# Kernel tuning notes

Measured on AMD Instinct MI355X. Metric: run time of the kernel, lower is better.

## Reference

```python
import jax, jax.numpy as jnp
import numpy as np

N, E, H, G, L = 50000, 640000, 128, 8, 3

def setup_inputs() -> dict:
    key = jax.random.key(0)
    ks = jax.random.split(key, 10)
    s = 1.0 / np.sqrt(H)
    return {
        "x": jax.random.normal(ks[0], (N, H), jnp.float32),
        "query": jax.random.normal(ks[1], (G, H), jnp.float32),
        "Wl": jax.random.normal(ks[2], (L, H, H), jnp.float32) * s,
        "bl": jax.random.normal(ks[3], (L, H), jnp.float32) * s,
        "Wr": jax.random.normal(ks[4], (L, H, H), jnp.float32) * s,
        "Wlin": jax.random.normal(ks[5], (H, H), jnp.float32) * s,
        "blin": jax.random.normal(ks[6], (H,), jnp.float32) * s,
        "edge_index": jax.random.randint(ks[7], (2, E), 0, N, jnp.int64),
        "batch_vec": jnp.sort(jax.random.randint(ks[8], (N,), 0, G, jnp.int64)),
    }

def reference(x, query, Wl, bl, Wr, Wlin, blin, edge_index, batch_vec):
    src, dst = edge_index[0], edge_index[1]
    n = x.shape[0]
    for i in range(L):
        # SAGEConv(aggr='max'): gather neighbor feats, scatter-max to dst
        m = jax.ops.segment_max(x[src], dst, num_segments=n)  # [N,H]
        m = jnp.where(jnp.isfinite(m), m, 0.0)  # isolated nodes -> 0 (PyG)
        x = jax.nn.relu(m @ Wl[i].T + bl[i] + x @ Wr[i].T)
    x = x @ Wlin.T + blin  # encoder final linear
    # cosine scoring per graph, vectorized via batch_vec
    xn = x / jnp.linalg.norm(x, axis=1, keepdims=True).clip(1e-12)
    qn = query / jnp.linalg.norm(query, axis=1, keepdims=True).clip(1e-12)
    scores = jnp.sum(xn * qn[batch_vec], axis=1)  # [N]
    return scores
```

## Files before the change

### kernel.cpp

```cpp
#include <hip/hip_runtime.h>
#include <math.h>

#define H 128

typedef _Float16 half8 __attribute__((ext_vector_type(8)));
typedef float f32x16 __attribute__((ext_vector_type(16)));
typedef int int4v __attribute__((ext_vector_type(4)));

__device__ __forceinline__ half8 h8max(half8 a, half8 b) {
#if defined(__has_builtin) && __has_builtin(__builtin_elementwise_max)
    return __builtin_elementwise_max(a, b);
#else
    half8 r;
#pragma unroll
    for (int j = 0; j < 8; ++j) r[j] = a[j] > b[j] ? a[j] : b[j];
    return r;
#endif
}

__device__ __forceinline__ half8 h8shfl_xor(half8 v, int mask) {
    int4v iv;
    __builtin_memcpy(&iv, &v, 16);
#pragma unroll
    for (int j = 0; j < 4; ++j) iv[j] = __shfl_xor(iv[j], mask, 64);
    half8 r;
    __builtin_memcpy(&r, &iv, 16);
    return r;
}


__global__ __launch_bounds__(256) void scan_atomic(const int* __restrict__ deg,
                                                   int* __restrict__ offsets,
                                                   int* __restrict__ gcur, int N) {
    __shared__ int buf[256];
    __shared__ int sbase;
    int tid = threadIdx.x;
    int i = blockIdx.x * 256 + tid;
    int v = (i < N) ? deg[i] : 0;
    int incl = v;
    buf[tid] = v;
    __syncthreads();
#pragma unroll
    for (int off = 1; off < 256; off <<= 1) {
        int t = (tid >= off) ? buf[tid - off] : 0;
        __syncthreads();
        incl += t;
        buf[tid] = incl;
        __syncthreads();
    }
    if (tid == 255) sbase = atomicAdd(gcur, incl);
    __syncthreads();
    if (i < N) offsets[i] = sbase + incl - v;
}

__global__ __launch_bounds__(256) void fill_adj(const int* __restrict__ ei, int E,
                                                const int* __restrict__ offsets,
                                                int* __restrict__ cursor,
                                                int* __restrict__ adj) {
    int e = blockIdx.x * 256 + threadIdx.x;
    if (e < E) {
        int s = ei[e];
        int d = ei[E + e];
        int pos = atomicAdd(&cursor[d], 1);
        adj[offsets[d] + pos] = s;
    }
}


__global__ __launch_bounds__(256) void prep_all(
    const int* __restrict__ ei, int E, int* __restrict__ deg,
    const float* __restrict__ x, const float* __restrict__ query,
    const float* __restrict__ Wl, const float* __restrict__ Wr,
    const float* __restrict__ Wlin, _Float16* __restrict__ xh,
    _Float16* __restrict__ wimg, float* __restrict__ qn, int n8, int HB, int SB,
    int WB) {
    int b = blockIdx.x;
    int tid = threadIdx.x;
    if (b < HB) {
        int e = b * 256 + tid;
        if (e < E) atomicAdd(&deg[ei[E + e]], 1);
    } else if (b < HB + SB) {
        int i = (b - HB) * 256 + tid;
        if (i < n8) {
            const float4* x4 = (const float4*)x;
            float4 u = x4[(size_t)i * 2], v = x4[(size_t)i * 2 + 1];
            float f[8] = {u.x, u.y, u.z, u.w, v.x, v.y, v.z, v.w};
            half8 h;
#pragma unroll
            for (int j = 0; j < 8; ++j) h[j] = (_Float16)f[j];
            *(half8*)(xh + (size_t)i * 8) = h;
        }
    } else if (b < HB + SB + WB) {
        int gidx = (b - HB - SB) * 256 + tid;
        if (gidx < 7 * 2048) {
            int mat = gidx / 2048;
            int rem = gidx - mat * 2048;
            int n = rem >> 4;
            int g = rem & 15;
            const float* src = (mat == 6) ? Wlin
                             : ((mat & 1) ? Wr + (mat >> 1) * H * H
                                          : Wl + (mat >> 1) * H * H);
            const float* p = src + n * H + g * 8;
            half8 h, l;
#pragma unroll
            for (int j = 0; j < 8; ++j) {
                float v = p[j];
                _Float16 hh = (_Float16)v;
                h[j] = hh;
                l[j] = (_Float16)(v - (float)hh);
            }
            int kc4 = g >> 2, gpc = g & 3;
            int posB = (gpc + (n & 3) + ((n >> 2) & 3)) & 3;
            size_t base = (size_t)mat * 32768 + (size_t)kc4 * 8192 + n * 32 + posB * 8;
            *(half8*)(wimg + base) = h;
            *(half8*)(wimg + base + 4096) = l;
        }
    } else {
        int g = b - HB - SB - WB;
        __shared__ float part[4];
        float v = (tid < 128) ? query[g * H + tid] : 0.f;
        float ss = v * v;
#pragma unroll
        for (int off = 32; off > 0; off >>= 1) ss += __shfl_xor(ss, off, 64);
        if ((tid & 63) == 0) part[tid >> 6] = ss;
        __syncthreads();
        float tot = part[0] + part[1];
        if (tid < 128) qn[g * H + tid] = v / fmaxf(sqrtf(tot), 1e-12f);
    }
}


__global__ __launch_bounds__(256, 8) void layer_fused(
    const half8* __restrict__ Xh, const int* __restrict__ deg,
    const int* __restrict__ offsets, const int* __restrict__ adj,
    const _Float16* __restrict__ Bimg, const float* __restrict__ bias,
    _Float16* __restrict__ Yh, int N) {
    __shared__ __align__(16) _Float16 sU[4096];

    int tid = threadIdx.x;
    int w = tid >> 6;
    int lane = tid & 63;
    int l31 = lane & 31;
    int lhi = lane >> 5;
    int n0 = blockIdx.x * 32;

    {
        int sub = lane >> 4;
        int lf = lane & 15;
        const _Float16 ni = (_Float16)(-INFINITY);
        const half8 ninf = {ni, ni, ni, ni, ni, ni, ni, ni};
        const half8 hz = {(_Float16)0.f, (_Float16)0.f, (_Float16)0.f, (_Float16)0.f,
                          (_Float16)0.f, (_Float16)0.f, (_Float16)0.f, (_Float16)0.f};
        int nd = n0 + w * 8 + (lf & 7);
        int ndc = nd < N ? nd : N - 1;
        int e0v = offsets[ndc];
        int degv = (nd < N) ? deg[ndc] : 0;

        int dmx = degv;
#pragma unroll
        for (int off = 1; off <= 8; off <<= 1) {
            int t = __shfl_xor(dmx, off, 64);
            dmx = t > dmx ? t : dmx;
        }

        if (dmx <= 32) {
            int adjf[4];
#pragma unroll
            for (int rr = 0; rr < 4; ++rr) {
                int i = 2 * rr + (lane >> 5);
                int e0 = __shfl(e0v, i, 64);
                int d = __shfl(degv, i, 64);
                int s = lane & 31;
                int p = d > 0 ? e0 + (s < d ? s : d - 1) : 0;
                adjf[rr] = adj[p];
            }
#pragma unroll
            for (int i = 0; i < 8; ++i) {
                int d = __shfl(degv, i, 64);
                int dm1 = d > 0 ? d - 1 : 0;
                half8 v[8];
#pragma unroll
                for (int q = 0; q < 8; ++q) {
                    int j = q * 4 + sub;
                    int jc = j < d ? j : dm1;
                    int idx = __shfl(adjf[i >> 1], ((i & 1) << 5) | jc, 64);
                    v[q] = Xh[(size_t)idx * 16 + lf];
                }
                half8 acc = h8max(h8max(h8max(v[0], v[1]), h8max(v[2], v[3])),
                                  h8max(h8max(v[4], v[5]), h8max(v[6], v[7])));
                acc = h8max(acc, h8shfl_xor(acc, 16));
                acc = h8max(acc, h8shfl_xor(acc, 32));
                if (d == 0) acc = hz;
                int row = w * 8 + i;
                if (sub == 0) *(half8*)&sU[row * 128 + ((lf ^ (row & 15)) << 3)] = acc;
            }
        } else {
            for (int i = 0; i < 8; ++i) {
                int e0 = __shfl(e0v, i, 64);
                int d = __shfl(degv, i, 64);
                int row = w * 8 + i;
                half8 acc = ninf;
                for (int base = 0; base < d; base += 16) {
                    half8 v[4];
#pragma unroll
                    for (int q = 0; q < 4; ++q) {
                        int j = base + q * 4 + sub;
                        int idx = adj[e0 + (j < d ? j : d - 1)];
                        v[q] = Xh[(size_t)idx * 16 + lf];
                    }
                    acc = h8max(acc, h8max(h8max(v[0], v[1]), h8max(v[2], v[3])));
                }
                acc = h8max(acc, h8shfl_xor(acc, 16));
                acc = h8max(acc, h8shfl_xor(acc, 32));
                if (d == 0) acc = hz;
                if (sub == 0) *(half8*)&sU[row * 128 + ((lf ^ (row & 15)) << 3)] = acc;
            }
        }
    }
    __syncthreads();

    f32x16 acc;
    {
        float bvv = bias[w * 32 + l31];
#pragma unroll
        for (int r = 0; r < 16; ++r) acc[r] = bvv;
    }

    int rl = l31;
    int n = w * 32 + l31;

#pragma unroll
    for (int kc4 = 0; kc4 < 4; ++kc4) {
        const _Float16* Bc = Bimg + (size_t)kc4 * 8192;
#pragma unroll
        for (int ks = 0; ks < 2; ++ks) {
            int g16 = kc4 * 4 + ks * 2 + lhi;
            int posA = g16 ^ (rl & 15);
            half8 ah = *(const half8*)&sU[rl * 128 + posA * 8];
            int gpc = ks * 2 + lhi;
            int posB = (gpc + (n & 3) + ((n >> 2) & 3)) & 3;
            half8 bh = *(const half8*)&Bc[n * 32 + posB * 8];
            half8 bl2 = *(const half8*)&Bc[4096 + n * 32 + posB * 8];
            acc = __builtin_amdgcn_mfma_f32_32x32x16_f16(ah, bh, acc, 0, 0, 0);
            acc = __builtin_amdgcn_mfma_f32_32x32x16_f16(ah, bl2, acc, 0, 0, 0);
        }
    }

#pragma unroll
    for (int kc64 = 0; kc64 < 2; ++kc64) {
        __syncthreads();
        {
            int row = tid >> 3;
            int gp8 = tid & 7;
            int nn = n0 + row;
            half8 h = {(_Float16)0.f, (_Float16)0.f, (_Float16)0.f, (_Float16)0.f,
                       (_Float16)0.f, (_Float16)0.f, (_Float16)0.f, (_Float16)0.f};
            if (nn < N) h = Xh[(size_t)nn * 16 + kc64 * 8 + gp8];
            int pos8 = (gp8 + (row & 7) + ((row >> 3) & 7)) & 7;
            *(half8*)&sU[row * 72 + pos8 * 8] = h;
        }
        __syncthreads();
#pragma unroll
        for (int kc4 = 2 * kc64; kc4 < 2 * kc64 + 2; ++kc4) {
            const _Float16* Bc = Bimg + 32768 + (size_t)kc4 * 8192;
#pragma unroll
            for (int ks = 0; ks < 2; ++ks) {
                int gp8 = (kc4 & 1) * 4 + ks * 2 + lhi;
                int posA8 = (gp8 + (rl & 7) + ((rl >> 3) & 7)) & 7;
                half8 ah = *(const half8*)&sU[rl * 72 + posA8 * 8];
                int gpc = ks * 2 + lhi;
                int posB = (gpc + (n & 3) + ((n >> 2) & 3)) & 3;
                half8 bh = *(const half8*)&Bc[n * 32 + posB * 8];
                half8 bl2 = *(const half8*)&Bc[4096 + n * 32 + posB * 8];
                acc = __builtin_amdgcn_mfma_f32_32x32x16_f16(ah, bh, acc, 0, 0, 0);
                acc = __builtin_amdgcn_mfma_f32_32x32x16_f16(ah, bl2, acc, 0, 0, 0);
            }
        }
    }

#pragma unroll
    for (int r = 0; r < 16; ++r) {
        int row = n0 + (r & 3) + 8 * (r >> 2) + 4 * lhi;
        if (row < N) Yh[(size_t)row * H + n] = (_Float16)fmaxf(acc[r], 0.f);
    }
}


__global__ __launch_bounds__(256) void final_mfma6(
    const half8* __restrict__ Xh, const _Float16* __restrict__ Bimg,
    const float* __restrict__ blin, const float* __restrict__ qn,
    const int* __restrict__ bv, float* __restrict__ out, int N) {
    __shared__ __align__(16) _Float16 sA[9216];
    __shared__ __align__(16) _Float16 sB[8192];

    int tid = threadIdx.x;
    int w = tid >> 6;
    int lane = tid & 63;
    int l31 = lane & 31;
    int lhi = lane >> 5;
    int n0 = blockIdx.x * 128;

    int arow = n0 + w * 32 + l31;
    arow = arow < N ? arow : N - 1;
    int gl = bv[arow];

    f32x16 acc[4];
#pragma unroll
    for (int nt = 0; nt < 4; ++nt) {
        float b = blin[nt * 32 + l31];
#pragma unroll
        for (int r = 0; r < 16; ++r) acc[nt][r] = b;
    }

    int rl = w * 32 + l31;

    for (int kc4 = 0; kc4 < 4; ++kc4) {
        if (kc4) __syncthreads();
        {
            const half8* bsrc = (const half8*)(Bimg + (size_t)kc4 * 8192);
            half8* bdst = (half8*)sB;
#pragma unroll
            for (int i = 0; i < 4; ++i) bdst[tid + i * 256] = bsrc[tid + i * 256];
        }
        if ((kc4 & 1) == 0) {
            int kc64 = kc4 >> 1;
#pragma unroll
            for (int i = 0; i < 4; ++i) {
                int idx = tid + i * 256;
                int row = idx >> 3;
                int gp8 = idx & 7;
                int nn = n0 + row;
                half8 h = {(_Float16)0.f, (_Float16)0.f, (_Float16)0.f, (_Float16)0.f,
                           (_Float16)0.f, (_Float16)0.f, (_Float16)0.f, (_Float16)0.f};
                if (nn < N) h = Xh[(size_t)nn * 16 + kc64 * 8 + gp8];
                int pos8 = (gp8 + (row & 7) + ((row >> 3) & 7)) & 7;
                *(half8*)&sA[row * 72 + pos8 * 8] = h;
            }
        }
        __syncthreads();
#pragma unroll
        for (int ks = 0; ks < 2; ++ks) {
            int gp8 = (kc4 & 1) * 4 + ks * 2 + lhi;
            int posA8 = (gp8 + (rl & 7) + ((rl >> 3) & 7)) & 7;
            half8 ah = *(const half8*)&sA[rl * 72 + posA8 * 8];
#pragma unroll
            for (int nt = 0; nt < 4; ++nt) {
                int nn = nt * 32 + l31;
                int gpc = ks * 2 + lhi;
                int posB = (gpc + (nn & 3) + ((nn >> 2) & 3)) & 3;
                half8 bh = *(const half8*)&sB[nn * 32 + posB * 8];
                half8 bl2 = *(const half8*)&sB[4096 + nn * 32 + posB * 8];
                acc[nt] = __builtin_amdgcn_mfma_f32_32x32x16_f16(ah, bh, acc[nt], 0, 0, 0);
                acc[nt] = __builtin_amdgcn_mfma_f32_32x32x16_f16(ah, bl2, acc[nt], 0, 0, 0);
            }
        }
    }

#pragma unroll
    for (int r = 0; r < 16; ++r) {
        int rloc = (r & 3) + 8 * (r >> 2) + 4 * lhi;
        int row = n0 + w * 32 + rloc;
        int g = __shfl(gl, rloc, 32);
        float ss = 0.f, sd = 0.f;
#pragma unroll
        for (int nt = 0; nt < 4; ++nt) {
            float y = acc[nt][r];
            float q = qn[(size_t)g * H + nt * 32 + l31];
            ss = fmaf(y, y, ss);
            sd = fmaf(y, q, sd);
        }
#pragma unroll
        for (int off = 1; off <= 16; off <<= 1) {
            ss += __shfl_xor(ss, off, 64);
            sd += __shfl_xor(sd, off, 64);
        }
        if (l31 == 0 && row < N) out[row] = sd / fmaxf(sqrtf(ss), 1e-12f);
    }
}


extern "C" void kernel_launch(void* const* d_in, const int* in_sizes, int n_in,
                              void* d_out, int out_size, void* d_ws, size_t ws_size,
                              hipStream_t stream) {
    const float* x = (const float*)d_in[0];
    const float* query = (const float*)d_in[1];
    const float* Wl = (const float*)d_in[2];
    const float* bl = (const float*)d_in[3];
    const float* Wr = (const float*)d_in[4];
    const float* Wlin = (const float*)d_in[5];
    const float* blin = (const float*)d_in[6];
    const int* ei = (const int*)d_in[7];
    const int* bv = (const int*)d_in[8];
    float* out = (float*)d_out;

    const int N = in_sizes[0] / H;
    const int E = in_sizes[7] / 2;
    const int G = in_sizes[1] / H;

    char* p = (char*)d_ws;
    auto alloc = [&](size_t bytes) {
        char* r = p;
        p += (bytes + 255) & ~(size_t)255;
        return r;
    };
    int* deg = (int*)alloc((size_t)(2 * N + 1) * sizeof(int));
    int* cursor = deg + N;
    int* gcur = deg + 2 * N;
    int* offsets = (int*)alloc((size_t)N * sizeof(int));
    int* adj = (int*)alloc((size_t)E * sizeof(int));
    float* qn = (float*)alloc((size_t)G * H * sizeof(float));
    _Float16* wimg = (_Float16*)alloc((size_t)7 * 32768 * sizeof(_Float16));
    size_t actH = (size_t)N * H * sizeof(_Float16);
    _Float16* xah = (_Float16*)alloc(actH);
    _Float16* xbh = (_Float16*)alloc(actH);

    hipMemsetAsync(deg, 0, (size_t)(2 * N + 1) * sizeof(int), stream);

    const int n8 = N * H / 8;
    const int HB = (E + 255) / 256;
    const int SB = (n8 + 255) / 256;
    const int WB = (7 * 2048 + 255) / 256;
    prep_all<<<HB + SB + WB + G, 256, 0, stream>>>(ei, E, deg, x, query, Wl, Wr,
                                                   Wlin, xah, wimg, qn, n8, HB,
                                                   SB, WB);
    scan_atomic<<<(N + 255) / 256, 256, 0, stream>>>(deg, offsets, gcur, N);
    fill_adj<<<(E + 255) / 256, 256, 0, stream>>>(ei, E, offsets, cursor, adj);

    const int NGm = (N + 31) / 32;
    const int NGf = (N + 127) / 128;

    layer_fused<<<NGm, 256, 0, stream>>>(
        (const half8*)xah, deg, offsets, adj, wimg + (size_t)0 * 65536,
        bl + 0 * H, xbh, N);
    layer_fused<<<NGm, 256, 0, stream>>>(
        (const half8*)xbh, deg, offsets, adj, wimg + (size_t)1 * 65536,
        bl + 1 * H, xah, N);
    layer_fused<<<NGm, 256, 0, stream>>>(
        (const half8*)xah, deg, offsets, adj, wimg + (size_t)2 * 65536,
        bl + 2 * H, xbh, N);
    final_mfma6<<<NGf, 256, 0, stream>>>(
        (const half8*)xbh, wimg + (size_t)6 * 32768, blin, qn, bv, out, N);
}
```

Baseline: 272.7 us.

## Repack weight image per lane, stage full X tile, skip upper neighbor gathers

Weight images for the SAGE layers are re-laid out so each lane's hi/lo fp16 fragments sit contiguously at lane*16, which turns the B-operand loads into sequential per-lane accesses. The self-term X tile is now staged once into a second LDS buffer, replacing two staged halves with extra barriers. The low-degree gather path skips the second set of four neighbor loads when degree is at most 16. Together these aim to reduce global load overhead, barriers and wasted gathers, at the cost of 8KB more shared memory per block, which may lower occupancy.

Result: no change. 268.6 us (-1.5%).

```diff
diff --git a/kernel.cpp b/kernel.cpp
--- a/kernel.cpp
+++ b/kernel.cpp
@@ -95,25 +95,50 @@
         if (gidx < 7 * 2048) {
             int mat = gidx / 2048;
             int rem = gidx - mat * 2048;
-            int n = rem >> 4;
-            int g = rem & 15;
-            const float* src = (mat == 6) ? Wlin
-                             : ((mat & 1) ? Wr + (mat >> 1) * H * H
-                                          : Wl + (mat >> 1) * H * H);
-            const float* p = src + n * H + g * 8;
-            half8 h, l;
-#pragma unroll
-            for (int j = 0; j < 8; ++j) {
-                float v = p[j];
-                _Float16 hh = (_Float16)v;
-                h[j] = hh;
-                l[j] = (_Float16)(v - (float)hh);
-            }
-            int kc4 = g >> 2, gpc = g & 3;
-            int posB = (gpc + (n & 3) + ((n >> 2) & 3)) & 3;
-            size_t base = (size_t)mat * 32768 + (size_t)kc4 * 8192 + n * 32 + posB * 8;
-            *(half8*)(wimg + base) = h;
-            *(half8*)(wimg + base + 4096) = l;
+            if (mat == 6) {
+                int n = rem >> 4;
+                int g = rem & 15;
+                const float* p = Wlin + n * H + g * 8;
+                half8 h, l;
+#pragma unroll
+                for (int j = 0; j < 8; ++j) {
+                    float v = p[j];
+                    _Float16 hh = (_Float16)v;
+                    h[j] = hh;
+                    l[j] = (_Float16)(v - (float)hh);
+                }
+                int kc4 = g >> 2, gpc = g & 3;
+                int posB = (gpc + (n & 3) + ((n >> 2) & 3)) & 3;
+                size_t base =
+                    (size_t)mat * 32768 + (size_t)kc4 * 8192 + n * 32 + posB * 8;
+                *(half8*)(wimg + base) = h;
+                *(half8*)(wimg + base + 4096) = l;
+            } else {
+                int kc4 = rem >> 9;
+                int r2 = rem & 511;
+                int s = r2 >> 6;
+                int lane = r2 & 63;
+                int ks = s >> 2;
+                int colgrp = s & 3;
+                int lhi = lane >> 5, l31 = lane & 31;
+                int n = colgrp * 32 + l31;
+                int g16 = kc4 * 4 + ks * 2 + lhi;
+                const float* src = (mat & 1) ? Wr + (mat >> 1) * H * H
+                                             : Wl + (mat >> 1) * H * H;
+                const float* p = src + n * H + g16 * 8;
+                half8 h, l;
+#pragma unroll
+                for (int j = 0; j < 8; ++j) {
+                    float v = p[j];
+                    _Float16 hh = (_Float16)v;
+                    h[j] = hh;
+                    l[j] = (_Float16)(v - (float)hh);
+                }
+                size_t base = (size_t)mat * 32768 + (size_t)kc4 * 8192 +
+                              (size_t)s * 1024 + (size_t)lane * 16;
+                *(half8*)(wimg + base) = h;
+                *(half8*)(wimg + base + 8) = l;
+            }
         }
     } else {
         int g = b - HB - SB - WB;
@@ -136,6 +161,7 @@
     const _Float16* __restrict__ Bimg, const float* __restrict__ bias,
     _Float16* __restrict__ Yh, int N) {
     __shared__ __align__(16) _Float16 sU[4096];
+    __shared__ __align__(16) _Float16 sX[4096];
 
     int tid = threadIdx.x;
     int w = tid >> 6;
@@ -178,16 +204,29 @@
             for (int i = 0; i < 8; ++i) {
                 int d = __shfl(degv, i, 64);
                 int dm1 = d > 0 ? d - 1 : 0;
-                half8 v[8];
-#pragma unroll
-                for (int q = 0; q < 8; ++q) {
-                    int j = q * 4 + sub;
-                    int jc = j < d ? j : dm1;
-                    int idx = __shfl(adjf[i >> 1], ((i & 1) << 5) | jc, 64);
-                    v[q] = Xh[(size_t)idx * 16 + lf];
+                int srcb = (i & 1) << 5;
+                int j0 = sub, j1 = 4 + sub, j2 = 8 + sub, j3 = 12 + sub;
+                int i0 = __shfl(adjf[i >> 1], srcb | (j0 < d ? j0 : dm1), 64);
+                int i1 = __shfl(adjf[i >> 1], srcb | (j1 < d ? j1 : dm1), 64);
+                int i2 = __shfl(adjf[i >> 1], srcb | (j2 < d ? j2 : dm1), 64);
+                int i3 = __shfl(adjf[i >> 1], srcb | (j3 < d ? j3 : dm1), 64);
+                half8 v0 = Xh[(size_t)i0 * 16 + lf];
+                half8 v1 = Xh[(size_t)i1 * 16 + lf];
+                half8 v2 = Xh[(size_t)i2 * 16 + lf];
+                half8 v3 = Xh[(size_t)i3 * 16 + lf];
+                half8 acc = h8max(h8max(v0, v1), h8max(v2, v3));
+                if (d > 16) {
+                    int j4 = 16 + sub, j5 = 20 + sub, j6 = 24 + sub, j7 = 28 + sub;
+                    int i4 = __shfl(adjf[i >> 1], srcb | (j4 < d ? j4 : dm1), 64);
+                    int i5 = __shfl(adjf[i >> 1], srcb | (j5 < d ? j5 : dm1), 64);
+                    int i6 = __shfl(adjf[i >> 1], srcb | (j6 < d ? j6 : dm1), 64);
+                    int i7 = __shfl(adjf[i >> 1], srcb | (j7 < d ? j7 : dm1), 64);
+                    half8 u0 = Xh[(size_t)i4 * 16 + lf];
+                    half8 u1 = Xh[(size_t)i5 * 16 + lf];
+                    half8 u2 = Xh[(size_t)i6 * 16 + lf];
+                    half8 u3 = Xh[(size_t)i7 * 16 + lf];
+                    acc = h8max(acc, h8max(h8max(u0, u1), h8max(u2, u3)));
                 }
-                half8 acc = h8max(h8max(h8max(v[0], v[1]), h8max(v[2], v[3])),
-                                  h8max(h8max(v[4], v[5]), h8max(v[6], v[7])));
                 acc = h8max(acc, h8shfl_xor(acc, 16));
                 acc = h8max(acc, h8shfl_xor(acc, 32));
                 if (d == 0) acc = hz;
@@ -219,6 +258,21 @@
     }
     __syncthreads();
 
+    {
+        const half8 hz = {(_Float16)0.f, (_Float16)0.f, (_Float16)0.f, (_Float16)0.f,
+                          (_Float16)0.f, (_Float16)0.f, (_Float16)0.f, (_Float16)0.f};
+#pragma unroll
+        for (int t = 0; t < 2; ++t) {
+            int idx = tid + t * 256;
+            int row = idx >> 4;
+            int g = idx & 15;
+            int nn = n0 + row;
+            half8 h = hz;
+            if (nn < N) h = Xh[(size_t)nn * 16 + g];
+            *(half8*)&sX[row * 128 + ((g ^ (row & 15)) << 3)] = h;
+        }
+    }
+
     f32x16 acc;
     {
         float bvv = bias[w * 32 + l31];
@@ -227,57 +281,43 @@
     }
 
     int rl = l31;
-    int n = w * 32 + l31;
 
 #pragma unroll
     for (int kc4 = 0; kc4 < 4; ++kc4) {
-        const _Float16* Bc = Bimg + (size_t)kc4 * 8192;
 #pragma unroll
         for (int ks = 0; ks < 2; ++ks) {
             int g16 = kc4 * 4 + ks * 2 + lhi;
             int posA = g16 ^ (rl & 15);
             half8 ah = *(const half8*)&sU[rl * 128 + posA * 8];
-            int gpc = ks * 2 + lhi;
-            int posB = (gpc + (n & 3) + ((n >> 2) & 3)) & 3;
-            half8 bh = *(const half8*)&Bc[n * 32 + posB * 8];
-            half8 bl2 = *(const half8*)&Bc[4096 + n * 32 + posB * 8];
+            size_t boff =
+                (size_t)kc4 * 8192 + (size_t)(ks * 4 + w) * 1024 + (size_t)lane * 16;
+            half8 bh = *(const half8*)&Bimg[boff];
+            half8 bl2 = *(const half8*)&Bimg[boff + 8];
             acc = __builtin_amdgcn_mfma_f32_32x32x16_f16(ah, bh, acc, 0, 0, 0);
             acc = __builtin_amdgcn_mfma_f32_32x32x16_f16(ah, bl2, acc, 0, 0, 0);
         }
     }
 
-#pragma unroll
-    for (int kc64 = 0; kc64 < 2; ++kc64) {
-        __syncthreads();
-        {
-            int row = tid >> 3;
-            int gp8 = tid & 7;
-            int nn = n0 + row;
-            half8 h = {(_Float16)0.f, (_Float16)0.f, (_Float16)0.f, (_Float16)0.f,
-                       (_Float16)0.f, (_Float16)0.f, (_Float16)0.f, (_Float16)0.f};
-            if (nn < N) h = Xh[(size_t)nn * 16 + kc64 * 8 + gp8];
-            int pos8 = (gp8 + (row & 7) + ((row >> 3) & 7)) & 7;
-            *(half8*)&sU[row * 72 + pos8 * 8] = h;
-        }
-        __syncthreads();
-#pragma unroll
-        for (int kc4 = 2 * kc64; kc4 < 2 * kc64 + 2; ++kc4) {
-            const _Float16* Bc = Bimg + 32768 + (size_t)kc4 * 8192;
-#pragma unroll
-            for (int ks = 0; ks < 2; ++ks) {
-                int gp8 = (kc4 & 1) * 4 + ks * 2 + lhi;
-                int posA8 = (gp8 + (rl & 7) + ((rl >> 3) & 7)) & 7;
-                half8 ah = *(const half8*)&sU[rl * 72 + posA8 * 8];
-                int gpc = ks * 2 + lhi;
-                int posB = (gpc + (n & 3) + ((n >> 2) & 3)) & 3;
-                half8 bh = *(const half8*)&Bc[n * 32 + posB * 8];
-                half8 bl2 = *(const half8*)&Bc[4096 + n * 32 + posB * 8];
-                acc = __builtin_amdgcn_mfma_f32_32x32x16_f16(ah, bh, acc, 0, 0, 0);
-                acc = __builtin_amdgcn_mfma_f32_32x32x16_f16(ah, bl2, acc, 0, 0, 0);
-            }
-        }
-    }
-
+    __syncthreads();
+
+    const _Float16* Br = Bimg + 32768;
+#pragma unroll
+    for (int kc4 = 0; kc4 < 4; ++kc4) {
+#pragma unroll
+        for (int ks = 0; ks < 2; ++ks) {
+            int g16 = kc4 * 4 + ks * 2 + lhi;
+            int posA = g16 ^ (rl & 15);
+            half8 ah = *(const half8*)&sX[rl * 128 + posA * 8];
+            size_t boff =
+                (size_t)kc4 * 8192 + (size_t)(ks * 4 + w) * 1024 + (size_t)lane * 16;
+            half8 bh = *(const half8*)&Br[boff];
+            half8 bl2 = *(const half8*)&Br[boff + 8];
+            acc = __builtin_amdgcn_mfma_f32_32x32x16_f16(ah, bh, acc, 0, 0, 0);
+            acc = __builtin_amdgcn_mfma_f32_32x32x16_f16(ah, bl2, acc, 0, 0, 0);
+        }
+    }
+
+    int n = w * 32 + l31;
 #pragma unroll
     for (int r = 0; r < 16; ++r) {
         int row = n0 + (r & 3) + 8 * (r >> 2) + 4 * lhi;
```
